# Optimization experiments

Measured on AMD Instinct MI355X. Metric: run time of the kernel, lower is better.

Reference implementation:

```python
import jax, jax.numpy as jnp
import numpy as np
import math

N_NODES = 50000
N_EDGES = 800000
IN_FEATS = 128
HID = 64
OUT = 2
D = 2  # num_layers


def calc_thetas(d):
    """Beta-distribution polynomial coefficients (ascending order), matching
    sympy.poly((x/2)**i * (1-x/2)**(d-i) / Beta(i+1, d+1-i)) with inverted coeffs."""
    thetas = []
    for i in range(d + 1):
        p1 = np.zeros(i + 1)
        p1[-1] = 0.5 ** i  # (x/2)^i, ascending coeffs
        p2 = np.array([math.comb(d - i, j) * (-0.5) ** j for j in range(d - i + 1)])  # (1-x/2)^(d-i)
        beta = math.factorial(i) * math.factorial(d - i) / math.factorial(d + 1)
        thetas.append((np.convolve(p1, p2) / beta).tolist())
    return thetas


def poly_branch(h, src, dst, thetas):
    """Run all PolyConv filters on activated features h; concat along feature dim."""
    n = h.shape[0]
    deg = jnp.zeros((n,), h.dtype).at[dst].add(jnp.ones((dst.shape[0],), h.dtype))
    dinv = jnp.clip(deg, 1.0, None) ** -0.5  # D^{-1/2} of in-degrees, clamped min 1
    dinv = dinv[:, None]
    outs = []
    for th in thetas:
        f = h
        acc = th[0] * h
        for k in range(1, len(th)):
            # feat <- feat - D^{-1/2} A D^{-1/2} feat  (copy_u / sum aggregation)
            agg = jax.ops.segment_sum((f * dinv)[src], dst, num_segments=n)
            f = f - agg * dinv
            acc = acc + th[k] * f
        outs.append(acc)
    return jnp.concatenate(outs, axis=-1)


def setup_inputs() -> dict:
    key = jax.random.key(0)
    ks = jax.random.split(key, 12)
    inp = {
        "x": jax.random.normal(ks[0], (N_NODES, IN_FEATS), jnp.float32),
        "sim_x": jax.random.normal(ks[1], (N_NODES, IN_FEATS), jnp.float32),
        "src": jax.random.randint(ks[2], (N_EDGES,), 0, N_NODES, jnp.int32),
        "dst": jax.random.randint(ks[3], (N_EDGES,), 0, N_NODES, jnp.int32),
        "sim_src": jax.random.randint(ks[4], (N_EDGES,), 0, N_NODES, jnp.int32),
        "sim_dst": jax.random.randint(ks[5], (N_EDGES,), 0, N_NODES, jnp.int32),
        "W1_o": jax.random.normal(ks[6], (IN_FEATS, HID), jnp.float32) / np.sqrt(IN_FEATS),
        "b1_o": jnp.zeros((HID,), jnp.float32),
        "W1_s": jax.random.normal(ks[7], (IN_FEATS, HID), jnp.float32) / np.sqrt(IN_FEATS),
        "b1_s": jnp.zeros((HID,), jnp.float32),
        "Wm1": jax.random.normal(ks[8], (HID * (D + 1) * 2, HID), jnp.float32) / np.sqrt(HID * (D + 1) * 2),
        "bm1": jnp.zeros((HID,), jnp.float32),
        "Wm2": jax.random.normal(ks[9], (HID, OUT), jnp.float32) / np.sqrt(HID),
        "bm2": jnp.zeros((OUT,), jnp.float32),
    }
    return inp


def reference(x, sim_x, src, dst, sim_src, sim_dst,
              W1_o, b1_o, W1_s, b1_s, Wm1, bm1, Wm2, bm2):
    thetas_o = calc_thetas(D)
    thetas_s = [[4.0] * (D + 1) for _ in range(D + 1)]  # conv_s uses constant theta=4

    h = jax.nn.relu(x @ W1_o + b1_o)
    h_final = poly_branch(h, src, dst, thetas_o)      # [N, HID*(D+1)]

    sh = jax.nn.relu(sim_x @ W1_s + b1_s)
    sim_h_final = poly_branch(sh, sim_src, sim_dst, thetas_s)

    h_all = jnp.concatenate([h_final, sim_h_final], axis=-1)  # [N, HID*(D+1)*2]
    logits = jax.nn.relu(h_all @ Wm1 + bm1) @ Wm2 + bm2
    return (h_all, logits)
```

## Files before the change

### kernel.cpp

```cpp
#include <hip/hip_runtime.h>
#include <hip/hip_fp16.h>


#define KB_BITS 10
#define KMAX 64
#define PCHUNK 4096
#define PVPT 16

__global__ __launch_bounds__(256) void bhist_kernel(
    const int* __restrict__ dst, const int* __restrict__ sim_dst,
    int* __restrict__ bhist, int E, int Es) {
    __shared__ int h[2 * KMAX];
    int tid = threadIdx.x;
    if (tid < 2 * KMAX) h[tid] = 0;
    __syncthreads();
    int total = E + Es;
    for (int e = blockIdx.x * 256 + tid; e < total; e += gridDim.x * 256) {
        if (e < E) atomicAdd(&h[dst[e] >> KB_BITS], 1);
        else       atomicAdd(&h[KMAX + (sim_dst[e - E] >> KB_BITS)], 1);
    }
    __syncthreads();
    if (tid < 2 * KMAX && h[tid]) atomicAdd(&bhist[tid], h[tid]);
}

__global__ __launch_bounds__(128) void bscan_kernel(
    const int* __restrict__ bhist, int* __restrict__ brow,
    int* __restrict__ gcur) {
    int g = threadIdx.x >> 6, lane = threadIdx.x & 63;
    int v = bhist[g * KMAX + lane];
    int inc = v;
    #pragma unroll
    for (int off = 1; off < 64; off <<= 1) {
        int u = __shfl_up(inc, off);
        if (lane >= off) inc += u;
    }
    int ex = inc - v;
    brow[g * (KMAX + 1) + lane] = ex;
    if (lane == 63) brow[g * (KMAX + 1) + KMAX] = inc;
    gcur[g * KMAX + lane] = ex;
}

__global__ __launch_bounds__(256) void partition_kernel(
    const int* __restrict__ src, const int* __restrict__ dst,
    const int* __restrict__ sim_src, const int* __restrict__ sim_dst,
    int* __restrict__ gcur, unsigned* __restrict__ staged,
    int E, int Es, int nbo) {
    int b = blockIdx.x;
    const int* S; const int* D; int Eg; int goff; unsigned* stg;
    if (b < nbo) { S = src; D = dst; Eg = E; goff = 0; stg = staged; }
    else { b -= nbo; S = sim_src; D = sim_dst; Eg = Es; goff = KMAX; stg = staged + E; }
    int e0 = b * PCHUNK;
    int cnt_blk = Eg - e0; if (cnt_blk > PCHUNK) cnt_blk = PCHUNK;
    __shared__ int hist[KMAX], basep[KMAX], cur[KMAX], gbase[KMAX];
    __shared__ unsigned srt[PCHUNK];
    int tid = threadIdx.x;
    if (tid < KMAX) hist[tid] = 0;
    __syncthreads();
    unsigned full[PVPT];
    #pragma unroll
    for (int i = 0; i < PVPT; ++i) {
        int idx = i * 256 + tid;
        if (idx < cnt_blk) {
            int e = e0 + idx;
            int d = D[e];
            unsigned bk = (unsigned)d >> KB_BITS;
            full[i] = (bk << 26) | ((unsigned)S[e] << KB_BITS) |
                      (unsigned)(d & ((1 << KB_BITS) - 1));
            atomicAdd(&hist[bk], 1);
        } else full[i] = 0xFFFFFFFFu;
    }
    __syncthreads();
    if (tid < 64) {
        int v = hist[tid];
        int inc = v;
        #pragma unroll
        for (int off = 1; off < 64; off <<= 1) {
            int u = __shfl_up(inc, off);
            if (tid >= off) inc += u;
        }
        int ex = inc - v;
        basep[tid] = ex;
        cur[tid] = ex;
        gbase[tid] = v ? atomicAdd(&gcur[goff + tid], v) : 0;
    }
    __syncthreads();
    #pragma unroll
    for (int i = 0; i < PVPT; ++i) {
        unsigned f = full[i];
        if (f != 0xFFFFFFFFu) {
            unsigned bk = f >> 26;
            int slot = atomicAdd(&cur[bk], 1);
            srt[slot] = f;
        }
    }
    __syncthreads();
    for (int slot = tid; slot < cnt_blk; slot += 256) {
        unsigned f = srt[slot];
        unsigned bk = f >> 26;
        int gpos = gbase[bk] + (slot - basep[bk]);
        stg[gpos] = f & 0x3FFFFFFu;
    }
}

__global__ __launch_bounds__(512) void place_kernel(
    const unsigned* __restrict__ staged, const int* __restrict__ brow,
    int* __restrict__ row_o, int* __restrict__ row_s,
    int* __restrict__ esrc_o, int* __restrict__ esrc_s,
    float* __restrict__ dinv, int N, int K, int E) {
    int b = blockIdx.x;
    const unsigned* stg; const int* br; int* row; int* esrc; float* dv;
    if (b < K) { stg = staged; br = brow; row = row_o; esrc = esrc_o; dv = dinv; }
    else { b -= K; stg = staged + E; br = brow + (KMAX + 1); row = row_s; esrc = esrc_s; dv = dinv + N; }
    int node0 = b << KB_BITS;
    int nn = N - node0; if (nn > (1 << KB_BITS)) nn = (1 << KB_BITS);
    int seg0 = br[b], seg1 = br[b + 1];
    __shared__ int ncnt[1 << KB_BITS];
    __shared__ int wsum[8];
    int tid = threadIdx.x;
    for (int i = tid; i < (1 << KB_BITS); i += 512) ncnt[i] = 0;
    __syncthreads();
    for (int j = seg0 + tid; j < seg1; j += 512)
        atomicAdd(&ncnt[stg[j] & ((1 << KB_BITS) - 1)], 1);
    __syncthreads();
    int i0 = tid * 2;
    int v0 = ncnt[i0], v1 = ncnt[i0 + 1];
    int s = v0 + v1;
    int inc = s;
    #pragma unroll
    for (int off = 1; off < 64; off <<= 1) {
        int u = __shfl_up(inc, off);
        if ((tid & 63) >= off) inc += u;
    }
    if ((tid & 63) == 63) wsum[tid >> 6] = inc;
    __syncthreads();
    int wo = 0;
    for (int w = 0; w < (tid >> 6); ++w) wo += wsum[w];
    int ex = seg0 + wo + inc - s;
    if (i0 < nn) {
        row[node0 + i0] = ex;
        dv[node0 + i0] = rsqrtf((float)(v0 > 1 ? v0 : 1));
    }
    if (i0 + 1 < nn) {
        row[node0 + i0 + 1] = ex + v0;
        dv[node0 + i0 + 1] = rsqrtf((float)(v1 > 1 ? v1 : 1));
    }
    if (b == K - 1 && tid == 0) row[N] = br[K];
    __syncthreads();
    ncnt[i0] = ex;
    ncnt[i0 + 1] = ex + v0;
    __syncthreads();
    for (int j = seg0 + tid; j < seg1; j += 512) {
        unsigned f = stg[j];
        int pos = atomicAdd(&ncnt[f & ((1 << KB_BITS) - 1)], 1);
        esrc[pos] = (int)(f >> KB_BITS);
    }
}

__global__ __launch_bounds__(256) void fold_kernel(
    const float* __restrict__ Wm1, float* __restrict__ w1f) {
    int i = blockIdx.x * 256 + threadIdx.x;
    if (i >= 256 * 64) return;
    int k = i >> 6, j = i & 63;
    float v = Wm1[k * 64 + j];
    if (k >= 192) v += Wm1[(k + 64) * 64 + j] + Wm1[(k + 128) * 64 + j];
    w1f[i] = v;
}

__global__ __launch_bounds__(256) void in_gemm_kernel(
    const float* __restrict__ x, const float* __restrict__ W,
    const float* __restrict__ b, float* __restrict__ out, int off,
    __half* __restrict__ h16, const float* __restrict__ dinvv, int n) {
    __shared__ float xs[64][132];
    __shared__ float Wf[128][68];
    int tid = threadIdx.x;
    int node0 = blockIdx.x * 64;
    const float4* wsrc = (const float4*)W;
    for (int i = tid; i < 2048; i += 256)
        *(float4*)&Wf[i >> 4][(i & 15) * 4] = wsrc[i];
    const float4* xsrc = (const float4*)x;
    for (int i = tid; i < 2048; i += 256) {
        int nl = i >> 5, c = i & 31;
        int node = node0 + nl;
        float4 v = make_float4(0.f, 0.f, 0.f, 0.f);
        if (node < n) v = xsrc[(long)node * 32 + c];
        *(float4*)&xs[nl][c * 4] = v;
    }
    __syncthreads();
    int tx = tid & 15, ty = tid >> 4;
    float acc[4][4] = {};
    #pragma unroll 2
    for (int k = 0; k < 128; k += 4) {
        float4 a[4], bb[4];
        #pragma unroll
        for (int i = 0; i < 4; ++i) a[i] = *(const float4*)&xs[ty * 4 + i][k];
        #pragma unroll
        for (int j = 0; j < 4; ++j) bb[j] = *(const float4*)&Wf[k + j][tx * 4];
        #pragma unroll
        for (int i = 0; i < 4; ++i) {
            acc[i][0] = fmaf(a[i].x, bb[0].x, acc[i][0]);
            acc[i][1] = fmaf(a[i].x, bb[0].y, acc[i][1]);
            acc[i][2] = fmaf(a[i].x, bb[0].z, acc[i][2]);
            acc[i][3] = fmaf(a[i].x, bb[0].w, acc[i][3]);
            acc[i][0] = fmaf(a[i].y, bb[1].x, acc[i][0]);
            acc[i][1] = fmaf(a[i].y, bb[1].y, acc[i][1]);
            acc[i][2] = fmaf(a[i].y, bb[1].z, acc[i][2]);
            acc[i][3] = fmaf(a[i].y, bb[1].w, acc[i][3]);
            acc[i][0] = fmaf(a[i].z, bb[2].x, acc[i][0]);
            acc[i][1] = fmaf(a[i].z, bb[2].y, acc[i][1]);
            acc[i][2] = fmaf(a[i].z, bb[2].z, acc[i][2]);
            acc[i][3] = fmaf(a[i].z, bb[2].w, acc[i][3]);
            acc[i][0] = fmaf(a[i].w, bb[3].x, acc[i][0]);
            acc[i][1] = fmaf(a[i].w, bb[3].y, acc[i][1]);
            acc[i][2] = fmaf(a[i].w, bb[3].z, acc[i][2]);
            acc[i][3] = fmaf(a[i].w, bb[3].w, acc[i][3]);
        }
    }
    float4 bias = *(const float4*)&b[tx * 4];
    #pragma unroll
    for (int i = 0; i < 4; ++i) {
        int node = node0 + ty * 4 + i;
        if (node >= n) break;
        float4 r;
        r.x = fmaxf(acc[i][0] + bias.x, 0.0f);
        r.y = fmaxf(acc[i][1] + bias.y, 0.0f);
        r.z = fmaxf(acc[i][2] + bias.z, 0.0f);
        r.w = fmaxf(acc[i][3] + bias.w, 0.0f);
        if (out) *(float4*)&out[(long)node * 384 + off + tx * 4] = r;
        if (h16) {
            float dvn = dinvv[node];
            __half hh[4];
            hh[0] = __float2half_rn(r.x * dvn);
            hh[1] = __float2half_rn(r.y * dvn);
            hh[2] = __float2half_rn(r.z * dvn);
            hh[3] = __float2half_rn(r.w * dvn);
            *(float2*)&h16[(long)node * 64 + tx * 4] = *(float2*)hh;
        }
    }
}

__global__ __launch_bounds__(256) void hop1_kernel(
    const int* __restrict__ row_o, const int* __restrict__ esrc_o,
    const int* __restrict__ row_s, const int* __restrict__ esrc_s,
    const __half* __restrict__ h16_o, const __half* __restrict__ h16_s,
    __half* __restrict__ g16_o, __half* __restrict__ g16_s,
    int n, int nb4) {
    int slot = blockIdx.x & 7;
    int g = slot >> 2;
    int bl = (blockIdx.x >> 3) * 4 + (slot & 3);
    if (bl >= nb4) return;
    const int* row; const int* esrc; const __half* h16; __half* g16;
    if (g == 0) { row = row_o; esrc = esrc_o; h16 = h16_o; g16 = g16_o; }
    else { row = row_s; esrc = esrc_s; h16 = h16_s; g16 = g16_s; }
    int d = bl * 4 + (threadIdx.x >> 6);
    if (d >= n) return;
    int lane = threadIdx.x & 63;
    int p = row[d], end = row[d + 1];
    int deg = end - p;
    float degf = (float)(deg > 1 ? deg : 1);
    float dd = rsqrtf(degf);
    float h16v = __half2float(h16[(long)d * 64 + lane]);
    float a0 = 0.f, a1 = 0.f, a2 = 0.f, a3 = 0.f;
    for (; p + 8 <= end; p += 8) {
        int s0 = esrc[p], s1 = esrc[p + 1], s2 = esrc[p + 2], s3 = esrc[p + 3];
        int s4 = esrc[p + 4], s5 = esrc[p + 5], s6 = esrc[p + 6], s7 = esrc[p + 7];
        a0 += __half2float(h16[(long)s0 * 64 + lane]);
        a1 += __half2float(h16[(long)s1 * 64 + lane]);
        a2 += __half2float(h16[(long)s2 * 64 + lane]);
        a3 += __half2float(h16[(long)s3 * 64 + lane]);
        a0 += __half2float(h16[(long)s4 * 64 + lane]);
        a1 += __half2float(h16[(long)s5 * 64 + lane]);
        a2 += __half2float(h16[(long)s6 * 64 + lane]);
        a3 += __half2float(h16[(long)s7 * 64 + lane]);
    }
    for (; p < end; ++p) {
        int s = esrc[p];
        a0 += __half2float(h16[(long)s * 64 + lane]);
    }
    float acc = (a0 + a1) + (a2 + a3);
    g16[(long)d * 64 + lane] = __float2half_rn(h16v - acc * dd * dd);
}

__global__ __launch_bounds__(256) void hop2_kernel(
    const int* __restrict__ row_o, const int* __restrict__ esrc_o,
    const int* __restrict__ row_s, const int* __restrict__ esrc_s,
    const __half* __restrict__ h16_o, const __half* __restrict__ h16_s,
    const __half* __restrict__ g16_o, const __half* __restrict__ g16_s,
    float* __restrict__ hall, int n, int nb4) {
    int slot = blockIdx.x & 7;
    int g = slot >> 2;
    int bl = (blockIdx.x >> 3) * 4 + (slot & 3);
    if (bl >= nb4) return;
    const int* row; const int* esrc; const __half* h16; const __half* g16; int base;
    if (g == 0) { row = row_o; esrc = esrc_o; h16 = h16_o; g16 = g16_o; base = 0; }
    else { row = row_s; esrc = esrc_s; h16 = h16_s; g16 = g16_s; base = 192; }
    int d = bl * 4 + (threadIdx.x >> 6);
    if (d >= n) return;
    int lane = threadIdx.x & 63;
    int p = row[d], end = row[d + 1];
    int deg = end - p;
    float degf = (float)(deg > 1 ? deg : 1);
    float dd = rsqrtf(degf);
    float sq = sqrtf(degf);
    float f0 = __half2float(h16[(long)d * 64 + lane]) * sq;
    float f1 = __half2float(g16[(long)d * 64 + lane]) * sq;
    float a0 = 0.f, a1 = 0.f, a2 = 0.f, a3 = 0.f;
    for (; p + 8 <= end; p += 8) {
        int s0 = esrc[p], s1 = esrc[p + 1], s2 = esrc[p + 2], s3 = esrc[p + 3];
        int s4 = esrc[p + 4], s5 = esrc[p + 5], s6 = esrc[p + 6], s7 = esrc[p + 7];
        a0 += __half2float(g16[(long)s0 * 64 + lane]);
        a1 += __half2float(g16[(long)s1 * 64 + lane]);
        a2 += __half2float(g16[(long)s2 * 64 + lane]);
        a3 += __half2float(g16[(long)s3 * 64 + lane]);
        a0 += __half2float(g16[(long)s4 * 64 + lane]);
        a1 += __half2float(g16[(long)s5 * 64 + lane]);
        a2 += __half2float(g16[(long)s6 * 64 + lane]);
        a3 += __half2float(g16[(long)s7 * 64 + lane]);
    }
    for (; p < end; ++p) {
        int s = esrc[p];
        a0 += __half2float(g16[(long)s * 64 + lane]);
    }
    float acc = (a0 + a1) + (a2 + a3);
    float f2 = f1 - acc * dd;
    long ob = (long)d * 384 + lane;
    if (g == 0) {
        hall[ob]       = 3.0f * f0 - 3.0f * f1 + 0.75f * f2;
        hall[ob + 64]  = 3.0f * f1 - 1.5f * f2;
        hall[ob + 128] = 0.75f * f2;
    } else {
        float ss = 4.0f * (f0 + f1 + f2);
        hall[ob + 192] = ss; hall[ob + 256] = ss; hall[ob + 320] = ss;
    }
}

__global__ __launch_bounds__(256) void gather2_kernel(
    const int* __restrict__ row_o, const int* __restrict__ esrc_o, const float* __restrict__ dinv_o,
    const int* __restrict__ row_s, const int* __restrict__ esrc_s, const float* __restrict__ dinv_s,
    float* __restrict__ hall, int in_off_o, int in_off_s, int n, int nb) {
    int b = blockIdx.x;
    const int* row; const int* esrc; const float* dinv; int in_off;
    if (b < nb) { row = row_o; esrc = esrc_o; dinv = dinv_o; in_off = in_off_o; }
    else { b -= nb; row = row_s; esrc = esrc_s; dinv = dinv_s; in_off = in_off_s; }
    int d = b * 4 + (threadIdx.x >> 6);
    if (d >= n) return;
    int lane = threadIdx.x & 63;
    int p = row[d], end = row[d + 1];
    const float* fin = hall + in_off;
    float a0 = 0.f, a1 = 0.f, a2 = 0.f, a3 = 0.f;
    for (; p + 4 <= end; p += 4) {
        int s0 = esrc[p], s1 = esrc[p + 1], s2 = esrc[p + 2], s3 = esrc[p + 3];
        a0 = fmaf(fin[(long)s0 * 384 + lane], dinv[s0], a0);
        a1 = fmaf(fin[(long)s1 * 384 + lane], dinv[s1], a1);
        a2 = fmaf(fin[(long)s2 * 384 + lane], dinv[s2], a2);
        a3 = fmaf(fin[(long)s3 * 384 + lane], dinv[s3], a3);
    }
    for (; p < end; ++p) {
        int s = esrc[p];
        a0 = fmaf(fin[(long)s * 384 + lane], dinv[s], a0);
    }
    float acc = (a0 + a1) + (a2 + a3);
    long ob = (long)d * 384 + lane;
    hall[ob + in_off + 64] = fin[ob] - acc * dinv[d];
}

__global__ __launch_bounds__(256) void combine_kernel(float* __restrict__ h, int nf) {
    int i = blockIdx.x * 256 + threadIdx.x;
    if (i >= nf) return;
    long ob = (long)(i >> 6) * 384 + (i & 63);
    float f0v = h[ob], f1v = h[ob + 64], f2v = h[ob + 128];
    h[ob]       = 3.0f * f0v - 3.0f * f1v + 0.75f * f2v;
    h[ob + 64]  = 3.0f * f1v - 1.5f * f2v;
    h[ob + 128] = 0.75f * f2v;
    float ss = 4.0f * (h[ob + 192] + h[ob + 256] + h[ob + 320]);
    h[ob + 192] = ss; h[ob + 256] = ss; h[ob + 320] = ss;
}

__global__ __launch_bounds__(256) void mlp_kernel(
    const float* __restrict__ hall, const float* __restrict__ w1f,
    const float* __restrict__ bm1, const float* __restrict__ Wm2,
    const float* __restrict__ bm2, float* __restrict__ logits, int n) {
    __shared__ float xs[64][132];
    __shared__ float Wf[128][68];
    int tid = threadIdx.x;
    int node0 = blockIdx.x * 64;
    int tx = tid & 15, ty = tid >> 4;
    float acc[4][4] = {};
    const float4* wsrc = (const float4*)w1f;
    const float4* hsrc = (const float4*)hall;
    for (int c = 0; c < 2; ++c) {
        __syncthreads();
        for (int i = tid; i < 2048; i += 256)
            *(float4*)&Wf[i >> 4][(i & 15) * 4] = wsrc[c * 2048 + i];
        for (int i = tid; i < 2048; i += 256) {
            int nl = i >> 5, cc = i & 31;
            int node = node0 + nl;
            float4 v = make_float4(0.f, 0.f, 0.f, 0.f);
            if (node < n) v = hsrc[(long)node * 96 + c * 32 + cc];
            *(float4*)&xs[nl][cc * 4] = v;
        }
        __syncthreads();
        #pragma unroll 2
        for (int k = 0; k < 128; k += 4) {
            float4 a[4], bb[4];
            #pragma unroll
            for (int i = 0; i < 4; ++i) a[i] = *(const float4*)&xs[ty * 4 + i][k];
            #pragma unroll
            for (int j = 0; j < 4; ++j) bb[j] = *(const float4*)&Wf[k + j][tx * 4];
            #pragma unroll
            for (int i = 0; i < 4; ++i) {
                acc[i][0] = fmaf(a[i].x, bb[0].x, acc[i][0]);
                acc[i][1] = fmaf(a[i].x, bb[0].y, acc[i][1]);
                acc[i][2] = fmaf(a[i].x, bb[0].z, acc[i][2]);
                acc[i][3] = fmaf(a[i].x, bb[0].w, acc[i][3]);
                acc[i][0] = fmaf(a[i].y, bb[1].x, acc[i][0]);
                acc[i][1] = fmaf(a[i].y, bb[1].y, acc[i][1]);
                acc[i][2] = fmaf(a[i].y, bb[1].z, acc[i][2]);
                acc[i][3] = fmaf(a[i].y, bb[1].w, acc[i][3]);
                acc[i][0] = fmaf(a[i].z, bb[2].x, acc[i][0]);
                acc[i][1] = fmaf(a[i].z, bb[2].y, acc[i][1]);
                acc[i][2] = fmaf(a[i].z, bb[2].z, acc[i][2]);
                acc[i][3] = fmaf(a[i].z, bb[2].w, acc[i][3]);
                acc[i][0] = fmaf(a[i].w, bb[3].x, acc[i][0]);
                acc[i][1] = fmaf(a[i].w, bb[3].y, acc[i][1]);
                acc[i][2] = fmaf(a[i].w, bb[3].z, acc[i][2]);
                acc[i][3] = fmaf(a[i].w, bb[3].w, acc[i][3]);
            }
        }
    }
    __syncthreads();
    float4 bias = *(const float4*)&bm1[tx * 4];
    #pragma unroll
    for (int i = 0; i < 4; ++i) {
        xs[ty * 4 + i][tx * 4 + 0] = fmaxf(acc[i][0] + bias.x, 0.0f);
        xs[ty * 4 + i][tx * 4 + 1] = fmaxf(acc[i][1] + bias.y, 0.0f);
        xs[ty * 4 + i][tx * 4 + 2] = fmaxf(acc[i][2] + bias.z, 0.0f);
        xs[ty * 4 + i][tx * 4 + 3] = fmaxf(acc[i][3] + bias.w, 0.0f);
    }
    __syncthreads();
    if (tid < 128) {
        int nl = tid >> 1, o = tid & 1;
        int node = node0 + nl;
        if (node < n) {
            float p = bm2[o];
            #pragma unroll 8
            for (int k = 0; k < 64; ++k) p = fmaf(xs[nl][k], Wm2[k * 2 + o], p);
            logits[(long)node * 2 + o] = p;
        }
    }
}

extern "C" void kernel_launch(void* const* d_in, const int* in_sizes, int n_in,
                              void* d_out, int out_size, void* d_ws, size_t ws_size,
                              hipStream_t stream) {
    const float* x     = (const float*)d_in[0];
    const float* sim_x = (const float*)d_in[1];
    const int* src     = (const int*)d_in[2];
    const int* dst     = (const int*)d_in[3];
    const int* sim_src = (const int*)d_in[4];
    const int* sim_dst = (const int*)d_in[5];
    const float* W1_o = (const float*)d_in[6];
    const float* b1_o = (const float*)d_in[7];
    const float* W1_s = (const float*)d_in[8];
    const float* b1_s = (const float*)d_in[9];
    const float* Wm1  = (const float*)d_in[10];
    const float* bm1  = (const float*)d_in[11];
    const float* Wm2  = (const float*)d_in[12];
    const float* bm2  = (const float*)d_in[13];

    const int N  = in_sizes[0] / 128;
    const int E  = in_sizes[2];
    const int Es = in_sizes[4];
    const int NF = N * 64;
    const int K  = (N + (1 << KB_BITS) - 1) >> KB_BITS;

    float* hall = (float*)d_out;
    float* lgt  = hall + (long)N * 384;
    float* dinv = lgt;
    float* dinv_o = dinv;
    float* dinv_s = dinv + N;

    int* row_o  = (int*)d_ws;
    int* row_s  = row_o + (N + 1);
    int* esrc_o = row_s + (N + 1);
    int* esrc_s = esrc_o + E;
    int* bhist  = esrc_s + Es;
    int* brow   = bhist + 2 * KMAX;
    int* gcur   = brow + 2 * (KMAX + 1);
    float* w1f  = (float*)(gcur + 2 * KMAX);
    __half* h16_o = (__half*)(w1f + 256 * 64);
    __half* h16_s = h16_o + (long)N * 64;
    __half* g16_o = h16_s + (long)N * 64;
    __half* g16_s = g16_o + (long)N * 64;
    size_t need_f16 = (size_t)((char*)(g16_s + (long)N * 64) - (char*)d_ws);
    bool f16path = ws_size >= need_f16;
    unsigned* staged = (unsigned*)h16_o;

    int nb4  = (N + 3) / 4;
    int nbq  = (nb4 + 3) / 4;
    int nb64 = (N + 63) / 64;
    int nfb  = (NF + 255) / 256;
    int nbo  = (E + PCHUNK - 1) / PCHUNK;
    int nbs  = (Es + PCHUNK - 1) / PCHUNK;

    hipMemsetAsync(bhist, 0, (size_t)(2 * KMAX) * sizeof(int), stream);
    fold_kernel<<<64, 256, 0, stream>>>(Wm1, w1f);
    bhist_kernel<<<256, 256, 0, stream>>>(dst, sim_dst, bhist, E, Es);
    bscan_kernel<<<1, 128, 0, stream>>>(bhist, brow, gcur);
    partition_kernel<<<nbo + nbs, 256, 0, stream>>>(src, dst, sim_src, sim_dst,
                                                    gcur, staged, E, Es, nbo);
    place_kernel<<<2 * K, 512, 0, stream>>>(staged, brow, row_o, row_s,
                                            esrc_o, esrc_s, dinv, N, K, E);

    in_gemm_kernel<<<nb64, 256, 0, stream>>>(x, W1_o, b1_o,
                                             f16path ? (float*)nullptr : hall, 0,
                                             f16path ? h16_o : (__half*)nullptr, dinv_o, N);
    in_gemm_kernel<<<nb64, 256, 0, stream>>>(sim_x, W1_s, b1_s,
                                             f16path ? (float*)nullptr : hall, 192,
                                             f16path ? h16_s : (__half*)nullptr, dinv_s, N);

    if (f16path) {
        hop1_kernel<<<nbq * 8, 256, 0, stream>>>(row_o, esrc_o, row_s, esrc_s,
                                                 h16_o, h16_s, g16_o, g16_s, N, nb4);
        hop2_kernel<<<nbq * 8, 256, 0, stream>>>(row_o, esrc_o, row_s, esrc_s,
                                                 h16_o, h16_s, g16_o, g16_s,
                                                 hall, N, nb4);
    } else {
        gather2_kernel<<<2 * nb4, 256, 0, stream>>>(row_o, esrc_o, dinv_o,
                                                    row_s, esrc_s, dinv_s,
                                                    hall, 0, 192, N, nb4);
        gather2_kernel<<<2 * nb4, 256, 0, stream>>>(row_o, esrc_o, dinv_o,
                                                    row_s, esrc_s, dinv_s,
                                                    hall, 64, 256, N, nb4);
        combine_kernel<<<nfb, 256, 0, stream>>>(hall, NF);
    }

    mlp_kernel<<<nb64, 256, 0, stream>>>(hall, w1f, bm1, Wm2, bm2, lgt, N);
}
```

Before: 411.8 us.

## Split wave into two half-groups gathering half2 per lane over alternating edges

In the hop1 and hop2 gather kernels, each 64-lane wave now covers a node with two 32-lane halves. Each lane loads a __half2 (two features) from a neighbour row, and the two halves take alternating edges, with a cross-half shuffle reduction at the end. This doubles bytes per load and halves the number of gather instructions per edge. Index and self-feature reads use nontemporal loads, and hop2 writes float2 outputs nontemporally, with the two halves splitting the output stores. The cost is an extra shuffle and more divergent handling of the odd tail edge.

Measured after the change: 445.9 us. +8.3%, slower.

```diff
diff --git a/kernel.cpp b/kernel.cpp
--- a/kernel.cpp
+++ b/kernel.cpp
@@ -6,6 +6,8 @@
 #define KMAX 64
 #define PCHUNK 4096
 #define PVPT 16
+
+typedef float f2_t __attribute__((ext_vector_type(2)));
 
 __global__ __launch_bounds__(256) void bhist_kernel(
     const int* __restrict__ dst, const int* __restrict__ sim_dst,
@@ -245,39 +247,50 @@
     __half* __restrict__ g16_o, __half* __restrict__ g16_s,
     int n, int nb4) {
     int slot = blockIdx.x & 7;
-    int g = slot >> 2;
+    int gg = slot >> 2;
     int bl = (blockIdx.x >> 3) * 4 + (slot & 3);
     if (bl >= nb4) return;
-    const int* row; const int* esrc; const __half* h16; __half* g16;
-    if (g == 0) { row = row_o; esrc = esrc_o; h16 = h16_o; g16 = g16_o; }
-    else { row = row_s; esrc = esrc_s; h16 = h16_s; g16 = g16_s; }
+    const int* row; const int* esrc; const __half2* h2; __half2* gout;
+    if (gg == 0) { row = row_o; esrc = esrc_o; h2 = (const __half2*)h16_o; gout = (__half2*)g16_o; }
+    else { row = row_s; esrc = esrc_s; h2 = (const __half2*)h16_s; gout = (__half2*)g16_s; }
     int d = bl * 4 + (threadIdx.x >> 6);
     if (d >= n) return;
     int lane = threadIdx.x & 63;
+    int g = lane >> 5, c = lane & 31;
     int p = row[d], end = row[d + 1];
     int deg = end - p;
     float degf = (float)(deg > 1 ? deg : 1);
     float dd = rsqrtf(degf);
-    float h16v = __half2float(h16[(long)d * 64 + lane]);
-    float a0 = 0.f, a1 = 0.f, a2 = 0.f, a3 = 0.f;
-    for (; p + 8 <= end; p += 8) {
-        int s0 = esrc[p], s1 = esrc[p + 1], s2 = esrc[p + 2], s3 = esrc[p + 3];
-        int s4 = esrc[p + 4], s5 = esrc[p + 5], s6 = esrc[p + 6], s7 = esrc[p + 7];
-        a0 += __half2float(h16[(long)s0 * 64 + lane]);
-        a1 += __half2float(h16[(long)s1 * 64 + lane]);
-        a2 += __half2float(h16[(long)s2 * 64 + lane]);
-        a3 += __half2float(h16[(long)s3 * 64 + lane]);
-        a0 += __half2float(h16[(long)s4 * 64 + lane]);
-        a1 += __half2float(h16[(long)s5 * 64 + lane]);
-        a2 += __half2float(h16[(long)s6 * 64 + lane]);
-        a3 += __half2float(h16[(long)s7 * 64 + lane]);
-    }
-    for (; p < end; ++p) {
+    float2 hv = __half22float2(h2[(long)d * 32 + c]);
+    float ax[4] = {0.f, 0.f, 0.f, 0.f}, ay[4] = {0.f, 0.f, 0.f, 0.f};
+    for (; p + 16 <= end; p += 16) {
+        int ss[8];
+        #pragma unroll
+        for (int i = 0; i < 8; ++i)
+            ss[i] = __builtin_nontemporal_load(esrc + p + 2 * i + g);
+        #pragma unroll
+        for (int i = 0; i < 8; ++i) {
+            float2 v = __half22float2(h2[(long)ss[i] * 32 + c]);
+            ax[i & 3] += v.x; ay[i & 3] += v.y;
+        }
+    }
+    for (; p + 2 <= end; p += 2) {
+        int s = __builtin_nontemporal_load(esrc + p + g);
+        float2 v = __half22float2(h2[(long)s * 32 + c]);
+        ax[0] += v.x; ay[0] += v.y;
+    }
+    if (p < end) {
         int s = esrc[p];
-        a0 += __half2float(h16[(long)s * 64 + lane]);
-    }
-    float acc = (a0 + a1) + (a2 + a3);
-    g16[(long)d * 64 + lane] = __float2half_rn(h16v - acc * dd * dd);
+        float2 v = __half22float2(h2[(long)s * 32 + c]);
+        if (!g) { ax[1] += v.x; ay[1] += v.y; }
+    }
+    float accx = (ax[0] + ax[1]) + (ax[2] + ax[3]);
+    float accy = (ay[0] + ay[1]) + (ay[2] + ay[3]);
+    accx += __shfl_xor(accx, 32);
+    accy += __shfl_xor(accy, 32);
+    float dd2 = dd * dd;
+    if (!g) gout[(long)d * 32 + c] = __floats2half2_rn(hv.x - accx * dd2,
+                                                       hv.y - accy * dd2);
 }
 
 __global__ __launch_bounds__(256) void hop2_kernel(
@@ -287,49 +300,74 @@
     const __half* __restrict__ g16_o, const __half* __restrict__ g16_s,
     float* __restrict__ hall, int n, int nb4) {
     int slot = blockIdx.x & 7;
-    int g = slot >> 2;
+    int gg = slot >> 2;
     int bl = (blockIdx.x >> 3) * 4 + (slot & 3);
     if (bl >= nb4) return;
-    const int* row; const int* esrc; const __half* h16; const __half* g16; int base;
-    if (g == 0) { row = row_o; esrc = esrc_o; h16 = h16_o; g16 = g16_o; base = 0; }
-    else { row = row_s; esrc = esrc_s; h16 = h16_s; g16 = g16_s; base = 192; }
+    const int* row; const int* esrc; const unsigned* h2u; const __half2* g2;
+    if (gg == 0) { row = row_o; esrc = esrc_o; h2u = (const unsigned*)h16_o; g2 = (const __half2*)g16_o; }
+    else { row = row_s; esrc = esrc_s; h2u = (const unsigned*)h16_s; g2 = (const __half2*)g16_s; }
     int d = bl * 4 + (threadIdx.x >> 6);
     if (d >= n) return;
     int lane = threadIdx.x & 63;
+    int g = lane >> 5, c = lane & 31;
     int p = row[d], end = row[d + 1];
     int deg = end - p;
     float degf = (float)(deg > 1 ? deg : 1);
     float dd = rsqrtf(degf);
     float sq = sqrtf(degf);
-    float f0 = __half2float(h16[(long)d * 64 + lane]) * sq;
-    float f1 = __half2float(g16[(long)d * 64 + lane]) * sq;
-    float a0 = 0.f, a1 = 0.f, a2 = 0.f, a3 = 0.f;
-    for (; p + 8 <= end; p += 8) {
-        int s0 = esrc[p], s1 = esrc[p + 1], s2 = esrc[p + 2], s3 = esrc[p + 3];
-        int s4 = esrc[p + 4], s5 = esrc[p + 5], s6 = esrc[p + 6], s7 = esrc[p + 7];
-        a0 += __half2float(g16[(long)s0 * 64 + lane]);
-        a1 += __half2float(g16[(long)s1 * 64 + lane]);
-        a2 += __half2float(g16[(long)s2 * 64 + lane]);
-        a3 += __half2float(g16[(long)s3 * 64 + lane]);
-        a0 += __half2float(g16[(long)s4 * 64 + lane]);
-        a1 += __half2float(g16[(long)s5 * 64 + lane]);
-        a2 += __half2float(g16[(long)s6 * 64 + lane]);
-        a3 += __half2float(g16[(long)s7 * 64 + lane]);
-    }
-    for (; p < end; ++p) {
+    unsigned h0u = __builtin_nontemporal_load(h2u + (long)d * 32 + c);
+    float2 f0v = __half22float2(*(__half2*)&h0u);
+    float2 f1v = __half22float2(g2[(long)d * 32 + c]);
+    float f0x = f0v.x * sq, f0y = f0v.y * sq;
+    float f1x = f1v.x * sq, f1y = f1v.y * sq;
+    float ax[4] = {0.f, 0.f, 0.f, 0.f}, ay[4] = {0.f, 0.f, 0.f, 0.f};
+    for (; p + 16 <= end; p += 16) {
+        int ss[8];
+        #pragma unroll
+        for (int i = 0; i < 8; ++i)
+            ss[i] = __builtin_nontemporal_load(esrc + p + 2 * i + g);
+        #pragma unroll
+        for (int i = 0; i < 8; ++i) {
+            float2 v = __half22float2(g2[(long)ss[i] * 32 + c]);
+            ax[i & 3] += v.x; ay[i & 3] += v.y;
+        }
+    }
+    for (; p + 2 <= end; p += 2) {
+        int s = __builtin_nontemporal_load(esrc + p + g);
+        float2 v = __half22float2(g2[(long)s * 32 + c]);
+        ax[0] += v.x; ay[0] += v.y;
+    }
+    if (p < end) {
         int s = esrc[p];
-        a0 += __half2float(g16[(long)s * 64 + lane]);
-    }
-    float acc = (a0 + a1) + (a2 + a3);
-    float f2 = f1 - acc * dd;
-    long ob = (long)d * 384 + lane;
-    if (g == 0) {
-        hall[ob]       = 3.0f * f0 - 3.0f * f1 + 0.75f * f2;
-        hall[ob + 64]  = 3.0f * f1 - 1.5f * f2;
-        hall[ob + 128] = 0.75f * f2;
+        float2 v = __half22float2(g2[(long)s * 32 + c]);
+        if (!g) { ax[1] += v.x; ay[1] += v.y; }
+    }
+    float accx = (ax[0] + ax[1]) + (ax[2] + ax[3]);
+    float accy = (ay[0] + ay[1]) + (ay[2] + ay[3]);
+    accx += __shfl_xor(accx, 32);
+    accy += __shfl_xor(accy, 32);
+    float f2x = f1x - accx * dd;
+    float f2y = f1y - accy * dd;
+    float* obp = hall + (long)d * 384 + c * 2;
+    if (gg == 0) {
+        f2_t o0 = {3.0f * f0x - 3.0f * f1x + 0.75f * f2x,
+                   3.0f * f0y - 3.0f * f1y + 0.75f * f2y};
+        f2_t o1 = {3.0f * f1x - 1.5f * f2x, 3.0f * f1y - 1.5f * f2y};
+        f2_t o2 = {0.75f * f2x, 0.75f * f2y};
+        if (!g) {
+            __builtin_nontemporal_store(o0, (f2_t*)obp);
+            __builtin_nontemporal_store(o2, (f2_t*)(obp + 128));
+        } else {
+            __builtin_nontemporal_store(o1, (f2_t*)(obp + 64));
+        }
     } else {
-        float ss = 4.0f * (f0 + f1 + f2);
-        hall[ob + 192] = ss; hall[ob + 256] = ss; hall[ob + 320] = ss;
+        f2_t ssv = {4.0f * (f0x + f1x + f2x), 4.0f * (f0y + f1y + f2y)};
+        if (!g) {
+            __builtin_nontemporal_store(ssv, (f2_t*)(obp + 192));
+            __builtin_nontemporal_store(ssv, (f2_t*)(obp + 320));
+        } else {
+            __builtin_nontemporal_store(ssv, (f2_t*)(obp + 256));
+        }
     }
 }
 
```
